# Optimization experiments

Hardware: AMD Instinct MI355X
Metric: run time of the kernel (lower is better)

Reference implementation:

```python
import jax, jax.numpy as jnp
import numpy as np

N_NODES = 50000
N_EDGES = 800000
IN_CH = 64
OUT_CH = 32
HEADS = 4
NEG_SLOPE = 0.2
EPS = 1e-16


def setup_inputs() -> dict:
    key = jax.random.key(0)
    ks = jax.random.split(key, 9)
    return {
        "x": jax.random.normal(ks[0], (N_NODES, IN_CH), dtype=jnp.float32),
        "edge_attr": jax.random.normal(ks[1], (N_EDGES, IN_CH), dtype=jnp.float32),
        "W": jax.random.normal(ks[2], (HEADS * OUT_CH, IN_CH), dtype=jnp.float32) * 0.1,
        "W_edge": jax.random.normal(ks[3], (HEADS * OUT_CH, IN_CH), dtype=jnp.float32) * 0.1,
        "att_src": jax.random.normal(ks[4], (HEADS, OUT_CH), dtype=jnp.float32) * 0.1,
        "att_dst": jax.random.normal(ks[5], (HEADS, OUT_CH), dtype=jnp.float32) * 0.1,
        "att_edge": jax.random.normal(ks[6], (HEADS, OUT_CH), dtype=jnp.float32) * 0.1,
        "bias_conv": jnp.zeros((OUT_CH,), dtype=jnp.float32),
        "bias_layer": jnp.zeros((OUT_CH,), dtype=jnp.float32),
        "edge_index": jax.random.randint(ks[7], (2, N_EDGES), 0, N_NODES, dtype=jnp.int32),
    }


def reference(x, edge_attr, W, W_edge, att_src, att_dst, att_edge, bias_conv, bias_layer, edge_index):
    # Node / edge linear projections -> [*, H, C]
    xh = (x @ W.T).reshape(-1, HEADS, OUT_CH)            # [N, H, C]
    eh = (edge_attr @ W_edge.T).reshape(-1, HEADS, OUT_CH)  # [E, H, C]

    src = edge_index[0]  # source nodes j (messages flow from)
    dst = edge_index[1]  # target nodes i (aggregation index)

    x_i = xh[dst]  # [E, H, C] target features
    x_j = xh[src]  # [E, H, C] source features

    # Attention logits per edge/head (matches CustomGATConv.message)
    alpha = (jnp.einsum('ehc,hc->eh', x_i, att_src)
             + jnp.einsum('ehc,hc->eh', x_j, att_dst)
             + jnp.einsum('ehc,hc->eh', eh, att_edge))  # [E, H]
    alpha = jax.nn.leaky_relu(alpha, NEG_SLOPE)

    # Segment softmax over edges grouped by target node
    seg_max = jax.ops.segment_max(alpha, dst, num_segments=N_NODES)  # [N, H]
    seg_max = jnp.where(jnp.isfinite(seg_max), seg_max, 0.0)
    alpha = jnp.exp(alpha - seg_max[dst])
    seg_sum = jax.ops.segment_sum(alpha, dst, num_segments=N_NODES)  # [N, H]
    alpha = alpha / (seg_sum[dst] + EPS)

    # Weighted scatter-add aggregation
    msg = x_j * alpha[:, :, None]  # [E, H, C]
    out = jax.ops.segment_sum(msg, dst, num_segments=N_NODES)  # [N, H, C]

    out = out.mean(axis=1) + bias_conv  # CustomGATConv: mean over heads + bias
    out = out + bias_layer              # SGATLayer bias (combine='mean' is no-op)
    return jax.nn.relu(out)
```

## Files before the change

### kernel.cpp

```cpp
#include <hip/hip_runtime.h>
#include <hip/hip_fp16.h>
#include <math.h>

#define N_NODES 50000
#define N_EDGES 800000
#define IN_CH 64
#define OUT_CH 32
#define HEADS 4
#define HC 128
#define NEG_SLOPE 0.2f
#define SOFT_EPS 1e-16f
#define CAP 48
#define NODE_BLOCKS 782

typedef _Float16 f16x4 __attribute__((ext_vector_type(4)));
typedef float    f32x4 __attribute__((ext_vector_type(4)));

__global__ __launch_bounds__(256) void k_node(const float* __restrict__ x,
                                              const float* __restrict__ W,
                                              const float* __restrict__ W_edge,
                                              const float* __restrict__ att_src,
                                              const float* __restrict__ att_dst,
                                              const float* __restrict__ att_edge,
                                              __half* __restrict__ xh16,
                                              float* __restrict__ a_src,
                                              float* __restrict__ a_dst,
                                              float* __restrict__ v_edge,
                                              int* __restrict__ cursor) {
    int tid = threadIdx.x;
    if (blockIdx.x == NODE_BLOCKS) {
        int h = tid >> 6, k = tid & 63;
        float s = 0.f;
        #pragma unroll
        for (int c = 0; c < OUT_CH; ++c)
            s += att_edge[h * OUT_CH + c] * W_edge[(h * OUT_CH + c) * IN_CH + k];
        v_edge[h * IN_CH + k] = s;
        return;
    }
    if (tid < 64) {
        int n0 = blockIdx.x * 64 + tid;
        if (n0 < N_NODES) cursor[n0] = 0;
    }

    int wv = tid >> 6, l = tid & 63;
    int g = l >> 4, r = l & 15;
    int tb = blockIdx.x * 64 + wv * 16;
    if (tb >= N_NODES) return;

    f16x4 wf[8][4];
    #pragma unroll
    for (int ot = 0; ot < 8; ++ot)
        #pragma unroll
        for (int kq = 0; kq < 4; ++kq) {
            float4 w4 = *(const float4*)(W + (ot * 16 + r) * IN_CH + kq * 16 + 4 * g);
            f16x4 f;
            f[0] = (_Float16)w4.x; f[1] = (_Float16)w4.y;
            f[2] = (_Float16)w4.z; f[3] = (_Float16)w4.w;
            wf[ot][kq] = f;
        }
    float asv[8], adv[8];
    #pragma unroll
    for (int ot = 0; ot < 8; ++ot) {
        asv[ot] = att_src[ot * 16 + r];
        adv[ot] = att_dst[ot * 16 + r];
    }
    f16x4 af[4];
    #pragma unroll
    for (int kq = 0; kq < 4; ++kq) {
        float4 x4 = *(const float4*)(x + (size_t)(tb + r) * IN_CH + kq * 16 + 4 * g);
        f16x4 f;
        f[0] = (_Float16)x4.x; f[1] = (_Float16)x4.y;
        f[2] = (_Float16)x4.z; f[3] = (_Float16)x4.w;
        af[kq] = f;
    }
    f32x4 acc[8];
    #pragma unroll
    for (int ot = 0; ot < 8; ++ot) acc[ot] = (f32x4){0.f, 0.f, 0.f, 0.f};
    #pragma unroll
    for (int kq = 0; kq < 4; ++kq)
        #pragma unroll
        for (int ot = 0; ot < 8; ++ot)
            acc[ot] = __builtin_amdgcn_mfma_f32_16x16x16f16(af[kq], wf[ot][kq],
                                                            acc[ot], 0, 0, 0);

    #pragma unroll
    for (int ot = 0; ot < 8; ++ot)
        #pragma unroll
        for (int reg = 0; reg < 4; ++reg) {
            int n = tb + g * 4 + reg;
            xh16[(size_t)n * HC + ot * 16 + r] = __float2half(acc[ot][reg]);
        }

    float ps[4][4], pd[4][4];
    #pragma unroll
    for (int reg = 0; reg < 4; ++reg)
        #pragma unroll
        for (int h = 0; h < 4; ++h) {
            ps[reg][h] = acc[2*h][reg] * asv[2*h] + acc[2*h+1][reg] * asv[2*h+1];
            pd[reg][h] = acc[2*h][reg] * adv[2*h] + acc[2*h+1][reg] * adv[2*h+1];
        }
    #pragma unroll
    for (int m = 1; m <= 8; m <<= 1)
        #pragma unroll
        for (int reg = 0; reg < 4; ++reg)
            #pragma unroll
            for (int h = 0; h < 4; ++h) {
                ps[reg][h] += __shfl_xor(ps[reg][h], m, 64);
                pd[reg][h] += __shfl_xor(pd[reg][h], m, 64);
            }
    if (r == 0) {
        #pragma unroll
        for (int reg = 0; reg < 4; ++reg) {
            int n = tb + g * 4 + reg;
            float4 vs = {ps[reg][0], ps[reg][1], ps[reg][2], ps[reg][3]};
            float4 vd = {pd[reg][0], pd[reg][1], pd[reg][2], pd[reg][3]};
            *(float4*)(a_src + n * 4) = vs;
            *(float4*)(a_dst + n * 4) = vd;
        }
    }
}

__global__ __launch_bounds__(256) void k_edge(const float* __restrict__ edge_attr,
                                              const int* __restrict__ srcI,
                                              const int* __restrict__ dstI,
                                              const float* __restrict__ v_edge,
                                              const float* __restrict__ a_src,
                                              const float* __restrict__ a_dst,
                                              int* __restrict__ cursor,
                                              uint4* __restrict__ perm) {
    __shared__ float vl[4 * IN_CH];
    int tid = threadIdx.x;
    vl[tid] = v_edge[tid];
    __syncthreads();
    int el = tid >> 2, part = tid & 3;
    size_t e = (size_t)blockIdx.x * 64 + el;
    if (e >= N_EDGES) return;

    int d = 0, s = 0, pl = 0;
    float4 as4 = {0, 0, 0, 0}, ad4 = {0, 0, 0, 0};
    if (part == 0) {
        d = dstI[e];
        s = srcI[e];
        pl = atomicAdd(&cursor[d], 1);
        as4 = ((const float4*)a_src)[d];
        ad4 = ((const float4*)a_dst)[s];
    }

    const float4* ea = (const float4*)(edge_attr + e * IN_CH + part * 16);
    float4 v0 = ea[0], v1 = ea[1], v2 = ea[2], v3 = ea[3];
    float p[4];
    #pragma unroll
    for (int h = 0; h < 4; ++h) {
        const float* vr = vl + h * IN_CH + part * 16;
        p[h] = v0.x * vr[0]  + v0.y * vr[1]  + v0.z * vr[2]  + v0.w * vr[3]
             + v1.x * vr[4]  + v1.y * vr[5]  + v1.z * vr[6]  + v1.w * vr[7]
             + v2.x * vr[8]  + v2.y * vr[9]  + v2.z * vr[10] + v2.w * vr[11]
             + v3.x * vr[12] + v3.y * vr[13] + v3.z * vr[14] + v3.w * vr[15];
    }
    #pragma unroll
    for (int h = 0; h < 4; ++h) {
        p[h] += __shfl_xor(p[h], 1, 64);
        p[h] += __shfl_xor(p[h], 2, 64);
    }
    if (part == 0 && pl < CAP) {
        float l0 = as4.x + ad4.x + p[0];
        float l1 = as4.y + ad4.y + p[1];
        float l2 = as4.z + ad4.z + p[2];
        float l3 = as4.w + ad4.w + p[3];
        l0 = l0 > 0.f ? l0 : NEG_SLOPE * l0;
        l1 = l1 > 0.f ? l1 : NEG_SLOPE * l1;
        l2 = l2 > 0.f ? l2 : NEG_SLOPE * l2;
        l3 = l3 > 0.f ? l3 : NEG_SLOPE * l3;
        __half2 w01 = __floats2half2_rn(__expf(l0), __expf(l1));
        __half2 w23 = __floats2half2_rn(__expf(l2), __expf(l3));
        uint4 rec;
        rec.x = *reinterpret_cast<unsigned int*>(&w01);
        rec.y = *reinterpret_cast<unsigned int*>(&w23);
        rec.z = (unsigned int)s;
        rec.w = 0u;
        perm[(size_t)d * CAP + pl] = rec;
    }
}

__device__ __forceinline__ float hget(unsigned int wbits, int odd) {
    __half2 h2 = *reinterpret_cast<__half2*>(&wbits);
    float2 f = __half22float2(h2);
    return odd ? f.y : f.x;
}

__global__ __launch_bounds__(256) void k_aggr(const uint4* __restrict__ perm,
                                              const int* __restrict__ cursor,
                                              const __half* __restrict__ xh16,
                                              const float* __restrict__ bias_conv,
                                              const float* __restrict__ bias_layer,
                                              float* __restrict__ out) {
    __shared__ uint4 recs[4][CAP];
    int w = threadIdx.x >> 6, l = threadIdx.x & 63;
    int i = blockIdx.x * 4 + w;
    if (i >= N_NODES) return;
    int cnt = cursor[i];
    cnt = cnt < CAP ? cnt : CAP;
    int h0 = l >> 4, odd = h0 & 1;

    const uint4* P = perm + (size_t)i * CAP;
    if (l < cnt) recs[w][l] = P[l];

    float s = 0.f, ax = 0.f, ay = 0.f;
    int j = 0;
    for (; j + 8 <= cnt; j += 8) {
        uint4 r0 = recs[w][j + 0], r1 = recs[w][j + 1];
        uint4 r2 = recs[w][j + 2], r3 = recs[w][j + 3];
        uint4 r4 = recs[w][j + 4], r5 = recs[w][j + 5];
        uint4 r6 = recs[w][j + 6], r7 = recs[w][j + 7];
        float2 f0 = __half22float2(((const __half2*)(xh16 + (size_t)r0.z * HC))[l]);
        float2 f1 = __half22float2(((const __half2*)(xh16 + (size_t)r1.z * HC))[l]);
        float2 f2 = __half22float2(((const __half2*)(xh16 + (size_t)r2.z * HC))[l]);
        float2 f3 = __half22float2(((const __half2*)(xh16 + (size_t)r3.z * HC))[l]);
        float2 f4 = __half22float2(((const __half2*)(xh16 + (size_t)r4.z * HC))[l]);
        float2 f5 = __half22float2(((const __half2*)(xh16 + (size_t)r5.z * HC))[l]);
        float2 f6 = __half22float2(((const __half2*)(xh16 + (size_t)r6.z * HC))[l]);
        float2 f7 = __half22float2(((const __half2*)(xh16 + (size_t)r7.z * HC))[l]);
        float w0 = hget(h0 < 2 ? r0.x : r0.y, odd);
        float w1 = hget(h0 < 2 ? r1.x : r1.y, odd);
        float w2 = hget(h0 < 2 ? r2.x : r2.y, odd);
        float w3 = hget(h0 < 2 ? r3.x : r3.y, odd);
        float w4 = hget(h0 < 2 ? r4.x : r4.y, odd);
        float w5 = hget(h0 < 2 ? r5.x : r5.y, odd);
        float w6 = hget(h0 < 2 ? r6.x : r6.y, odd);
        float w7 = hget(h0 < 2 ? r7.x : r7.y, odd);
        s  += ((w0 + w1) + (w2 + w3)) + ((w4 + w5) + (w6 + w7));
        ax += ((w0 * f0.x + w1 * f1.x) + (w2 * f2.x + w3 * f3.x))
            + ((w4 * f4.x + w5 * f5.x) + (w6 * f6.x + w7 * f7.x));
        ay += ((w0 * f0.y + w1 * f1.y) + (w2 * f2.y + w3 * f3.y))
            + ((w4 * f4.y + w5 * f5.y) + (w6 * f6.y + w7 * f7.y));
    }
    if (j + 4 <= cnt) {
        uint4 r0 = recs[w][j + 0], r1 = recs[w][j + 1];
        uint4 r2 = recs[w][j + 2], r3 = recs[w][j + 3];
        float2 f0 = __half22float2(((const __half2*)(xh16 + (size_t)r0.z * HC))[l]);
        float2 f1 = __half22float2(((const __half2*)(xh16 + (size_t)r1.z * HC))[l]);
        float2 f2 = __half22float2(((const __half2*)(xh16 + (size_t)r2.z * HC))[l]);
        float2 f3 = __half22float2(((const __half2*)(xh16 + (size_t)r3.z * HC))[l]);
        float w0 = hget(h0 < 2 ? r0.x : r0.y, odd);
        float w1 = hget(h0 < 2 ? r1.x : r1.y, odd);
        float w2 = hget(h0 < 2 ? r2.x : r2.y, odd);
        float w3 = hget(h0 < 2 ? r3.x : r3.y, odd);
        s  += (w0 + w1) + (w2 + w3);
        ax += (w0 * f0.x + w1 * f1.x) + (w2 * f2.x + w3 * f3.x);
        ay += (w0 * f0.y + w1 * f1.y) + (w2 * f2.y + w3 * f3.y);
        j += 4;
    }
    for (; j < cnt; ++j) {
        uint4 r0 = recs[w][j];
        float w0 = hget(h0 < 2 ? r0.x : r0.y, odd);
        float2 f0 = __half22float2(((const __half2*)(xh16 + (size_t)r0.z * HC))[l]);
        s  += w0;
        ax += w0 * f0.x;
        ay += w0 * f0.y;
    }
    float inv = 1.f / (s + SOFT_EPS);
    ax *= inv; ay *= inv;
    ax += __shfl_xor(ax, 16, 64); ax += __shfl_xor(ax, 32, 64);
    ay += __shfl_xor(ay, 16, 64); ay += __shfl_xor(ay, 32, 64);
    if (l < 16) {
        int c0 = 2 * l;
        float r0 = 0.25f * ax + bias_conv[c0]     + bias_layer[c0];
        float r1 = 0.25f * ay + bias_conv[c0 + 1] + bias_layer[c0 + 1];
        float2 o2 = {fmaxf(r0, 0.f), fmaxf(r1, 0.f)};
        ((float2*)(out + (size_t)i * OUT_CH))[l] = o2;
    }
}

extern "C" void kernel_launch(void* const* d_in, const int* in_sizes, int n_in,
                              void* d_out, int out_size, void* d_ws, size_t ws_size,
                              hipStream_t stream) {
    const float* x          = (const float*)d_in[0];
    const float* edge_attr  = (const float*)d_in[1];
    const float* W          = (const float*)d_in[2];
    const float* W_edge     = (const float*)d_in[3];
    const float* att_src    = (const float*)d_in[4];
    const float* att_dst    = (const float*)d_in[5];
    const float* att_edge   = (const float*)d_in[6];
    const float* bias_conv  = (const float*)d_in[7];
    const float* bias_layer = (const float*)d_in[8];
    const int*   edge_index = (const int*)d_in[9];
    const int* srcI = edge_index;
    const int* dstI = edge_index + N_EDGES;
    float* out = (float*)d_out;

    char* ws = (char*)d_ws;
    size_t off = 0;
    auto carve = [&](size_t bytes) -> char* {
        char* p = ws + off;
        off += (bytes + 255) & ~(size_t)255;
        return p;
    };
    __half* xh16  = (__half*)carve((size_t)N_NODES * HC * 2);
    uint4*  perm  = (uint4*)carve((size_t)N_NODES * CAP * 16);
    float* a_src  = (float*)carve((size_t)N_NODES * 4 * 4);
    float* a_dst  = (float*)carve((size_t)N_NODES * 4 * 4);
    float* v_edge = (float*)carve(4 * IN_CH * 4);
    int*   cursor = (int*)carve((size_t)N_NODES * 4);

    k_node<<<NODE_BLOCKS + 1, 256, 0, stream>>>(x, W, W_edge, att_src, att_dst,
                                                att_edge, xh16, a_src, a_dst,
                                                v_edge, cursor);
    k_edge<<<(N_EDGES + 63) / 64, 256, 0, stream>>>(edge_attr, srcI, dstI, v_edge,
                                                    a_src, a_dst, cursor, perm);
    k_aggr<<<(N_NODES + 3) / 4, 256, 0, stream>>>(perm, cursor, xh16,
                                                  bias_conv, bias_layer, out);
}
```

Baseline: 127.4 us.

## Fuse edge and aggregation kernels into one cooperative persistent kernel with grid sync

Merges the edge-scoring/bucketing kernel and the per-node aggregation kernel into a single cooperative launch. Persistent blocks loop over tiles, separated by a grid-wide barrier, and the old two-kernel path is kept as a fallback if the cooperative launch fails. The goal is to remove one kernel launch and its drain/ramp gap. In exchange it caps occupancy at what a cooperative launch allows, adds grid-sync cost, and makes host-side occupancy and attribute queries on every call.

```diff
diff --git a/kernel.cpp b/kernel.cpp
--- a/kernel.cpp
+++ b/kernel.cpp
@@ -1,6 +1,9 @@
 #include <hip/hip_runtime.h>
 #include <hip/hip_fp16.h>
+#include <hip/hip_cooperative_groups.h>
 #include <math.h>
+
+namespace cg = cooperative_groups;
 
 #define N_NODES 50000
 #define N_EDGES 800000
@@ -12,6 +15,8 @@
 #define SOFT_EPS 1e-16f
 #define CAP 48
 #define NODE_BLOCKS 782
+#define ETILES 12500
+#define ATILES 12500
 
 typedef _Float16 f16x4 __attribute__((ext_vector_type(4)));
 typedef float    f32x4 __attribute__((ext_vector_type(4)));
@@ -120,21 +125,23 @@
     }
 }
 
-__global__ __launch_bounds__(256) void k_edge(const float* __restrict__ edge_attr,
-                                              const int* __restrict__ srcI,
-                                              const int* __restrict__ dstI,
-                                              const float* __restrict__ v_edge,
-                                              const float* __restrict__ a_src,
-                                              const float* __restrict__ a_dst,
-                                              int* __restrict__ cursor,
-                                              uint4* __restrict__ perm) {
-    __shared__ float vl[4 * IN_CH];
-    int tid = threadIdx.x;
-    vl[tid] = v_edge[tid];
-    __syncthreads();
+__device__ __forceinline__ float hget(unsigned int wbits, int odd) {
+    __half2 h2 = *reinterpret_cast<__half2*>(&wbits);
+    float2 f = __half22float2(h2);
+    return odd ? f.y : f.x;
+}
+
+__device__ __forceinline__ void edge_tile(int t, int tid,
+                                          const float* __restrict__ edge_attr,
+                                          const int* __restrict__ srcI,
+                                          const int* __restrict__ dstI,
+                                          const float* vl,
+                                          const float* __restrict__ a_src,
+                                          const float* __restrict__ a_dst,
+                                          int* __restrict__ cursor,
+                                          uint4* __restrict__ perm) {
     int el = tid >> 2, part = tid & 3;
-    size_t e = (size_t)blockIdx.x * 64 + el;
-    if (e >= N_EDGES) return;
+    size_t e = (size_t)t * 64 + el;
 
     int d = 0, s = 0, pl = 0;
     float4 as4 = {0, 0, 0, 0}, ad4 = {0, 0, 0, 0};
@@ -182,22 +189,14 @@
     }
 }
 
-__device__ __forceinline__ float hget(unsigned int wbits, int odd) {
-    __half2 h2 = *reinterpret_cast<__half2*>(&wbits);
-    float2 f = __half22float2(h2);
-    return odd ? f.y : f.x;
-}
-
-__global__ __launch_bounds__(256) void k_aggr(const uint4* __restrict__ perm,
-                                              const int* __restrict__ cursor,
-                                              const __half* __restrict__ xh16,
-                                              const float* __restrict__ bias_conv,
-                                              const float* __restrict__ bias_layer,
-                                              float* __restrict__ out) {
-    __shared__ uint4 recs[4][CAP];
-    int w = threadIdx.x >> 6, l = threadIdx.x & 63;
-    int i = blockIdx.x * 4 + w;
-    if (i >= N_NODES) return;
+__device__ __forceinline__ void aggr_tile(int t, int w, int l, uint4 (*recs)[CAP],
+                                          const uint4* __restrict__ perm,
+                                          const int* __restrict__ cursor,
+                                          const __half* __restrict__ xh16,
+                                          const float* __restrict__ bias_conv,
+                                          const float* __restrict__ bias_layer,
+                                          float* __restrict__ out) {
+    int i = t * 4 + w;
     int cnt = cursor[i];
     cnt = cnt < CAP ? cnt : CAP;
     int h0 = l >> 4, odd = h0 & 1;
@@ -271,6 +270,62 @@
     }
 }
 
+__global__ __launch_bounds__(256) void k_ea(const float* __restrict__ edge_attr,
+                                            const int* __restrict__ srcI,
+                                            const int* __restrict__ dstI,
+                                            const float* __restrict__ v_edge,
+                                            const float* __restrict__ a_src,
+                                            const float* __restrict__ a_dst,
+                                            int* __restrict__ cursor,
+                                            uint4* __restrict__ perm,
+                                            const __half* __restrict__ xh16,
+                                            const float* __restrict__ bias_conv,
+                                            const float* __restrict__ bias_layer,
+                                            float* __restrict__ out) {
+    cg::grid_group grid = cg::this_grid();
+    __shared__ float vl[4 * IN_CH];
+    __shared__ uint4 recs[4][CAP];
+    int tid = threadIdx.x;
+    vl[tid] = v_edge[tid];
+    __syncthreads();
+    int nblk = gridDim.x;
+
+    for (int t = blockIdx.x; t < ETILES; t += nblk)
+        edge_tile(t, tid, edge_attr, srcI, dstI, vl, a_src, a_dst, cursor, perm);
+
+    grid.sync();
+
+    int w = tid >> 6, l = tid & 63;
+    for (int t = blockIdx.x; t < ATILES; t += nblk)
+        aggr_tile(t, w, l, recs, perm, cursor, xh16, bias_conv, bias_layer, out);
+}
+
+__global__ __launch_bounds__(256) void k_edge(const float* __restrict__ edge_attr,
+                                              const int* __restrict__ srcI,
+                                              const int* __restrict__ dstI,
+                                              const float* __restrict__ v_edge,
+                                              const float* __restrict__ a_src,
+                                              const float* __restrict__ a_dst,
+                                              int* __restrict__ cursor,
+                                              uint4* __restrict__ perm) {
+    __shared__ float vl[4 * IN_CH];
+    int tid = threadIdx.x;
+    vl[tid] = v_edge[tid];
+    __syncthreads();
+    edge_tile(blockIdx.x, tid, edge_attr, srcI, dstI, vl, a_src, a_dst, cursor, perm);
+}
+
+__global__ __launch_bounds__(256) void k_aggr(const uint4* __restrict__ perm,
+                                              const int* __restrict__ cursor,
+                                              const __half* __restrict__ xh16,
+                                              const float* __restrict__ bias_conv,
+                                              const float* __restrict__ bias_layer,
+                                              float* __restrict__ out) {
+    __shared__ uint4 recs[4][CAP];
+    int w = threadIdx.x >> 6, l = threadIdx.x & 63;
+    aggr_tile(blockIdx.x, w, l, recs, perm, cursor, xh16, bias_conv, bias_layer, out);
+}
+
 extern "C" void kernel_launch(void* const* d_in, const int* in_sizes, int n_in,
                               void* d_out, int out_size, void* d_ws, size_t ws_size,
                               hipStream_t stream) {
@@ -305,8 +360,30 @@
     k_node<<<NODE_BLOCKS + 1, 256, 0, stream>>>(x, W, W_edge, att_src, att_dst,
                                                 att_edge, xh16, a_src, a_dst,
                                                 v_edge, cursor);
-    k_edge<<<(N_EDGES + 63) / 64, 256, 0, stream>>>(edge_attr, srcI, dstI, v_edge,
-                                                    a_src, a_dst, cursor, perm);
-    k_aggr<<<(N_NODES + 3) / 4, 256, 0, stream>>>(perm, cursor, xh16,
-                                                  bias_conv, bias_layer, out);
-}
+
+    int dev = 0;
+    hipGetDevice(&dev);
+    int numCU = 0;
+    if (hipDeviceGetAttribute(&numCU, hipDeviceAttributeMultiprocessorCount, dev)
+            != hipSuccess || numCU <= 0)
+        numCU = 256;
+    int maxB = 0;
+    if (hipOccupancyMaxActiveBlocksPerMultiprocessor(&maxB, (const void*)k_ea,
+                                                     256, 0) != hipSuccess || maxB < 1)
+        maxB = 1;
+    long nblk = (long)maxB * numCU;
+    if (nblk > ETILES) nblk = ETILES;
+
+    void* args[] = { (void*)&edge_attr, (void*)&srcI, (void*)&dstI, (void*)&v_edge,
+                     (void*)&a_src, (void*)&a_dst, (void*)&cursor, (void*)&perm,
+                     (void*)&xh16, (void*)&bias_conv, (void*)&bias_layer,
+                     (void*)&out };
+    hipError_t err = hipLaunchCooperativeKernel((const void*)k_ea, dim3((int)nblk),
+                                                dim3(256), args, 0, stream);
+    if (err != hipSuccess) {
+        k_edge<<<ETILES, 256, 0, stream>>>(edge_attr, srcI, dstI, v_edge,
+                                           a_src, a_dst, cursor, perm);
+        k_aggr<<<ATILES, 256, 0, stream>>>(perm, cursor, xh16,
+                                           bias_conv, bias_layer, out);
+    }
+}
```

Result: slower. 240.2 us (+88.6%).
